# Optimization experiments

Measured on AMD Instinct MI355X. Metric: run time of the kernel, lower is better.

The kernel has to match this reference:

```python
import jax, jax.numpy as jnp
import numpy as np

N = 50000      # n_nodes
S = 16         # neighbors per node
D_IN = 256     # raw feature dim
PREP = 128     # prep_len
H = 2          # n_head
OUT = 64       # per-head spec output_dim (concat_node doubles it)
MP = 2         # n_mp (metapaths)
IN2 = 2 * OUT * H  # layer-2 input dim = 256


def setup_inputs() -> dict:
    key = jax.random.key(0)
    ks = jax.random.split(key, 7)
    feats = jax.random.normal(ks[0], (N, D_IN), jnp.float32)
    prep_W = jax.random.normal(ks[1], (D_IN, PREP), jnp.float32) * 0.05
    Wx1 = jax.random.normal(ks[2], (MP, H, PREP, OUT), jnp.float32) * 0.05
    Wn1 = jax.random.normal(ks[3], (MP, H, PREP, OUT), jnp.float32) * 0.05
    Wx2 = jax.random.normal(ks[4], (MP, H, IN2, OUT), jnp.float32) * 0.05
    Wn2 = jax.random.normal(ks[5], (MP, H, IN2, OUT), jnp.float32) * 0.05
    node_neigh = jax.random.randint(ks[6], (MP, N, S), 0, N, dtype=jnp.int32)
    return {"feats": feats, "prep_W": prep_W, "Wx1": Wx1, "Wn1": Wn1,
            "Wx2": Wx2, "Wn2": Wn2, "node_neigh": node_neigh}


def _agg_layer(x, neigh, Wx, Wn):
    # x: [N, d]; neigh: [N, S]; Wx, Wn: [H, d, OUT]
    # neighbor gather + mean (the chunk_edge = all_feats[node_neigh] path)
    agg = jnp.mean(x[neigh], axis=1)                  # [N, d]
    xh = jnp.einsum('nd,hdo->nho', x, Wx)             # [N, H, OUT]
    nh = jnp.einsum('nd,hdo->nho', agg, Wn)           # [N, H, OUT]
    h = jax.nn.relu(jnp.concatenate([xh, nh], -1))    # per-head concat_node
    return h.reshape(x.shape[0], -1)                  # heads concatenated


def reference(feats, prep_W, Wx1, Wn1, Wx2, Wn2, node_neigh):
    # feats[all_ids].detach() in the original -> stop_gradient
    feats = jax.lax.stop_gradient(feats)
    outs = []
    for mp in range(MP):
        h0 = feats @ prep_W                           # prep (dummy == layer-1 prep here)
        neigh = node_neigh[mp]
        h1 = _agg_layer(h0, neigh, Wx1[mp], Wn1[mp])  # [N, 256]
        h2 = _agg_layer(h1, neigh, Wx2[mp], Wn2[mp])  # [N, 256]
        outs.append(jnp.concatenate([h1, h2], axis=-1))  # skip-buffer concat
    return jnp.stack(outs, axis=0)                    # [MP, N, 512]
```

## Files before the change

kernel.cpp:

```cpp
#include <hip/hip_runtime.h>

#define NN 50000
#define SNEI 16
#define GB 782

typedef unsigned short ushort_t;
typedef unsigned int uint_t;
typedef unsigned long long u64;
typedef __attribute__((ext_vector_type(8))) short bhalf8;
typedef __attribute__((ext_vector_type(4))) float facc4;

__device__ __forceinline__ float b2f(uint_t u) {
    union { uint_t u; float f; } x; x.u = u << 16; return x.f;
}
__device__ __forceinline__ ushort_t f2b(float f) {
    union { float f; uint_t u; } x; x.f = f;
    return (ushort_t)((x.u + 0x7FFFu + ((x.u >> 16) & 1u)) >> 16);
}
__device__ __forceinline__ u64 pack4(float a, float b, float c, float d) {
    return (u64)f2b(a) | ((u64)f2b(b) << 16) | ((u64)f2b(c) << 32) | ((u64)f2b(d) << 48);
}

typedef const __attribute__((address_space(1))) void cglb_t;
typedef __attribute__((address_space(3))) void lds3_t;
__device__ __forceinline__ void gload16(const void* g, void* l) {
    __builtin_amdgcn_global_load_lds((cglb_t*)g, (lds3_t*)l, 16, 0, 0);
}

__global__ void permSetup(const float* __restrict__ prepW,
                          const float* __restrict__ Wx1, const float* __restrict__ Wn1,
                          const float* __restrict__ Wx2, const float* __restrict__ Wn2,
                          ushort_t* __restrict__ dst)
{
    int e = blockIdx.x * 256 + threadIdx.x;
    int q8 = e >> 3, j = e & 7;
    int layer = q8 >> 14;
    int qq = q8 & 16383;
    int mp = qq >> 13, isN = (qq >> 12) & 1, q = qq & 4095;
    int lane = q & 63, nf = (q >> 6) & 7, ks = q >> 9;
    int c = nf * 16 + (lane & 15);
    int k = ks * 32 + ((lane >> 4) << 3) + j;
    float v;
    if (layer == 0) {
        const float* W1 = (isN ? Wn1 : Wx1) + mp * 16384 + (c >> 6) * 8192 + (c & 63);
        const float* pw = prepW + (size_t)k * 128;
        float s = 0.f;
#pragma unroll 8
        for (int p = 0; p < 128; ++p) s += pw[p] * W1[(size_t)p * 64];
        v = s;
    } else {
        const float* W2 = (isN ? Wn2 : Wx2) + mp * 32768 + (c >> 6) * 16384 + (size_t)k * 64 + (c & 63);
        v = *W2;
    }
    dst[(size_t)q8 * 8 + j] = f2b(v);
}

template<bool XF32, bool L1>
__global__ __launch_bounds__(256, 4)
void proj_gemm(const void* __restrict__ Xv, size_t xStr,
               const ushort_t* __restrict__ W, size_t wStr,
               float* __restrict__ out, size_t oStr,
               ushort_t* __restrict__ h1, size_t hStr,
               ushort_t* __restrict__ P, size_t PStr)
{
    __shared__ bhalf8 lds[2560];
    u64* l64 = (u64*)lds;
    const int tid = threadIdx.x;
    const int lane = tid & 63;
    const int wid = tid >> 6;
    const int wave_m = wid >> 1, wave_n = wid & 1;
    const int m0 = blockIdx.x * 64;
    const int mp = blockIdx.y;

    const ushort_t* wx = W + (size_t)mp * wStr;
    const ushort_t* wn = wx + 4096 * 8;
    const float*    Xf = (const float*)Xv    + (size_t)mp * xStr;
    const ushort_t* Xb = (const ushort_t*)Xv + (size_t)mp * xStr;
    float* outp = out + (size_t)mp * oStr;
    ushort_t* h1p = L1 ? (h1 + (size_t)mp * hStr) : nullptr;
    ushort_t* Pp  = P + (size_t)mp * PStr;

    facc4 acc[2][8];
    const facc4 z = {0.f, 0.f, 0.f, 0.f};
#pragma unroll
    for (int i = 0; i < 2; ++i)
#pragma unroll
        for (int j = 0; j < 8; ++j) acc[i][j] = z;

    for (int kt = 0; kt < 4; ++kt) {
        if constexpr (XF32) {
#pragma unroll
            for (int it = 0; it < 2; ++it) {
                int s = tid + it * 256;
                int fp = s >> 6, ls = s & 63;
                int mf = fp & 3, ksl = fp >> 2;
                int grow = m0 + mf * 16 + (ls & 15); if (grow > NN - 1) grow = NN - 1;
                const float* gp = Xf + (size_t)grow * 256 + kt * 64 + ksl * 32 + ((ls >> 4) << 3);
                float4 f0 = *(const float4*)gp, f1 = *(const float4*)(gp + 4);
                l64[s * 2]     = pack4(f0.x, f0.y, f0.z, f0.w);
                l64[s * 2 + 1] = pack4(f1.x, f1.y, f1.z, f1.w);
            }
        } else {
#pragma unroll
            for (int it = 0; it < 2; ++it) {
                int u = wid + it * 4;
                int mf = u & 3, ksl = u >> 2;
                int grow = m0 + mf * 16 + (lane & 15); if (grow > NN - 1) grow = NN - 1;
                const ushort_t* src = Xb + (size_t)grow * 256 + kt * 64 + ksl * 32 + ((lane >> 4) << 3);
                gload16(src, (char*)lds + (u * 64 + lane) * 16);
            }
        }
#pragma unroll
        for (int it = 0; it < 4; ++it) {
            int cb = (it * 4 + wid) * 64;
            gload16(wx + ((size_t)kt * 1024 + cb + lane) * 8,
                    (char*)lds + (512 + cb + lane) * 16);
            gload16(wn + ((size_t)kt * 1024 + cb + lane) * 8,
                    (char*)lds + (1536 + cb + lane) * 16);
        }
        __syncthreads();
        const int wB = wave_n ? 1536 : 512;
#pragma unroll
        for (int ksl = 0; ksl < 2; ++ksl) {
            bhalf8 a0 = lds[(ksl * 4 + wave_m * 2 + 0) * 64 + lane];
            bhalf8 a1 = lds[(ksl * 4 + wave_m * 2 + 1) * 64 + lane];
#pragma unroll
            for (int nf = 0; nf < 8; ++nf) {
                bhalf8 b = lds[wB + (ksl * 8 + nf) * 64 + lane];
                acc[0][nf] = __builtin_amdgcn_mfma_f32_16x16x32_bf16(a0, b, acc[0][nf], 0, 0, 0);
                acc[1][nf] = __builtin_amdgcn_mfma_f32_16x16x32_bf16(a1, b, acc[1][nf], 0, 0, 0);
            }
        }
        __syncthreads();
    }
    const int cl = lane & 15, rg = lane >> 4;
    const int obase = L1 ? 0 : 256;
#pragma unroll
    for (int mf2 = 0; mf2 < 2; ++mf2) {
        int rowb = m0 + (wave_m * 2 + mf2) * 16 + rg * 4;
#pragma unroll
        for (int nf = 0; nf < 8; ++nf) {
            int cpr = nf * 16 + cl;
            int icol = (cpr >> 6) * 128 + (cpr & 63);
            facc4 v = acc[mf2][nf];
#pragma unroll
            for (int rr = 0; rr < 4; ++rr) {
                int row = rowb + rr;
                if (row < NN) {
                    if (wave_n == 0) {
                        float f = fmaxf(v[rr], 0.0f);
                        outp[(size_t)row * 512 + obase + icol] = f;
                        if constexpr (L1)
                            h1p[(size_t)row * 256 + icol] = f2b(f);
                    } else {
                        Pp[(size_t)row * 128 + cpr] = f2b(v[rr]);
                    }
                }
            }
        }
    }
}

template<bool L1>
__global__ __launch_bounds__(256)
void gatherK(const ushort_t* __restrict__ P, size_t PStr,
             const int* __restrict__ nb, size_t nStr,
             float* __restrict__ out, size_t oStr,
             ushort_t* __restrict__ h1, size_t hStr)
{
    const int mp = blockIdx.y;
    const ushort_t* Pp = P + (size_t)mp * PStr;
    const int* nbp = nb + (size_t)mp * nStr;
    float* outp = out + (size_t)mp * oStr;

    __shared__ int nls[256];
    const int nodeBase = blockIdx.x * 16;
    nls[threadIdx.x] = nbp[(size_t)nodeBase * SNEI + threadIdx.x];
    __syncthreads();

    const int nl = threadIdx.x >> 4, c = threadIdx.x & 15;
    const int node = nodeBase + nl;
    const int* nr = nls + nl * SNEI;
    float a0=0.f,a1=0.f,a2=0.f,a3=0.f,a4=0.f,a5=0.f,a6=0.f,a7=0.f;
#pragma unroll
    for (int s = 0; s < SNEI; ++s) {
        uint4 v = *(const uint4*)(Pp + (size_t)nr[s] * 128 + c * 8);
        a0 += b2f(v.x & 0xFFFFu); a1 += b2f(v.x >> 16);
        a2 += b2f(v.y & 0xFFFFu); a3 += b2f(v.y >> 16);
        a4 += b2f(v.z & 0xFFFFu); a5 += b2f(v.z >> 16);
        a6 += b2f(v.w & 0xFFFFu); a7 += b2f(v.w >> 16);
    }
    const float M = 0.0625f;
    float r0 = fmaxf(a0*M, 0.f), r1 = fmaxf(a1*M, 0.f);
    float r2 = fmaxf(a2*M, 0.f), r3 = fmaxf(a3*M, 0.f);
    float r4 = fmaxf(a4*M, 0.f), r5 = fmaxf(a5*M, 0.f);
    float r6 = fmaxf(a6*M, 0.f), r7 = fmaxf(a7*M, 0.f);
    const int head = c >> 3, off = (c & 7) * 8;
    const int obase = L1 ? 0 : 256;
    float* o = outp + (size_t)node * 512 + obase + head * 128 + 64 + off;
    *(float4*)o       = make_float4(r0, r1, r2, r3);
    *(float4*)(o + 4) = make_float4(r4, r5, r6, r7);
    if constexpr (L1) {
        ushort_t* hp = h1 + (size_t)mp * hStr + (size_t)node * 256 + head * 128 + 64 + off;
        *(u64*)hp       = pack4(r0, r1, r2, r3);
        *(u64*)(hp + 4) = pack4(r4, r5, r6, r7);
    }
}

extern "C" void kernel_launch(void* const* d_in, const int* in_sizes, int n_in,
                              void* d_out, int out_size, void* d_ws, size_t ws_size,
                              hipStream_t stream)
{
    const float* feats  = (const float*)d_in[0];
    const float* prepWp = (const float*)d_in[1];
    const float* Wx1    = (const float*)d_in[2];
    const float* Wn1    = (const float*)d_in[3];
    const float* Wx2    = (const float*)d_in[4];
    const float* Wn2    = (const float*)d_in[5];
    const int*   neigh  = (const int*)d_in[6];
    float* out = (float*)d_out;
    ushort_t* ws = (ushort_t*)d_ws;

    const size_t permElems = 262144;
    const size_t needBatched = permElems * 2
        + 2 * ((size_t)NN * 128 * 2 + (size_t)NN * 256 * 2);
    const bool batched = ws_size >= needBatched;
    const int nmp = batched ? 2 : 1;

    ushort_t* perm = ws;
    ushort_t* P    = ws + permElems;
    ushort_t* h1   = P + (size_t)nmp * NN * 128;

    permSetup<<<1024, 256, 0, stream>>>(prepWp, Wx1, Wn1, Wx2, Wn2, perm);

    const size_t PStr = batched ? (size_t)NN * 128 : 0;
    const size_t hStr = batched ? (size_t)NN * 256 : 0;
    const size_t oStr = batched ? (size_t)NN * 512 : 0;
    const size_t nStr = batched ? (size_t)NN * SNEI : 0;
    const size_t wStr = batched ? (size_t)8192 * 8 : 0;
    const int passes = batched ? 1 : 2;

    for (int p = 0; p < passes; ++p) {
        const ushort_t* w1 = perm + (size_t)p * 8192 * 8;
        const ushort_t* w2 = perm + (size_t)(16384 + p * 8192) * 8;
        float* outp = out + (size_t)p * NN * 512;
        const int* nbp = neigh + (size_t)p * NN * SNEI;
        dim3 gp(GB, nmp), gg(NN / 16, nmp);

        proj_gemm<true, true><<<gp, 256, 0, stream>>>(
            feats, 0, w1, wStr, outp, oStr, h1, hStr, P, PStr);
        gatherK<true><<<gg, 256, 0, stream>>>(
            P, PStr, nbp, nStr, outp, oStr, h1, hStr);
        proj_gemm<false, false><<<gp, 256, 0, stream>>>(
            h1, hStr, w2, wStr, outp, oStr, nullptr, 0, P, PStr);
        gatherK<false><<<gg, 256, 0, stream>>>(
            P, PStr, nbp, nStr, outp, oStr, nullptr, 0);
    }
}
```

Baseline: 193.2 us.

## Slice projected neighbor table by 32-column chunks for cache-friendlier gather

The projected neighbor features P are now stored as four column slices of 32 bf16 values per node instead of 128-wide rows. The gather kernel gets a slice grid dimension, so each block reads only 64-byte rows from one 3.2MB slice. That slice is more likely to stay resident in L2/LLC during the random neighbor gather. Each block now handles 64 nodes with a vectorized, clamped neighbor-index load, and the setup dot product uses two accumulators. The trade-off is that each neighbor index is read four times, once per slice, and output writes become narrower strided chunks.

```diff
diff --git a/kernel.cpp b/kernel.cpp
--- a/kernel.cpp
+++ b/kernel.cpp
@@ -44,10 +44,13 @@
     if (layer == 0) {
         const float* W1 = (isN ? Wn1 : Wx1) + mp * 16384 + (c >> 6) * 8192 + (c & 63);
         const float* pw = prepW + (size_t)k * 128;
-        float s = 0.f;
-#pragma unroll 8
-        for (int p = 0; p < 128; ++p) s += pw[p] * W1[(size_t)p * 64];
-        v = s;
+        float s0 = 0.f, s1 = 0.f;
+#pragma unroll 4
+        for (int p = 0; p < 128; p += 2) {
+            s0 += pw[p]     * W1[(size_t)p * 64];
+            s1 += pw[p + 1] * W1[(size_t)(p + 1) * 64];
+        }
+        v = s0 + s1;
     } else {
         const float* W2 = (isN ? Wn2 : Wx2) + mp * 32768 + (c >> 6) * 16384 + (size_t)k * 64 + (c & 63);
         v = *W2;
@@ -153,7 +156,7 @@
                         if constexpr (L1)
                             h1p[(size_t)row * 256 + icol] = f2b(f);
                     } else {
-                        Pp[(size_t)row * 128 + cpr] = f2b(v[rr]);
+                        Pp[(size_t)(cpr >> 5) * (NN * 32) + (size_t)row * 32 + (cpr & 31)] = f2b(v[rr]);
                     }
                 }
             }
@@ -163,28 +166,35 @@
 
 template<bool L1>
 __global__ __launch_bounds__(256)
-void gatherK(const ushort_t* __restrict__ P, size_t PStr,
+void gatherS(const ushort_t* __restrict__ P, size_t PStr,
              const int* __restrict__ nb, size_t nStr,
              float* __restrict__ out, size_t oStr,
              ushort_t* __restrict__ h1, size_t hStr)
 {
-    const int mp = blockIdx.y;
-    const ushort_t* Pp = P + (size_t)mp * PStr;
+    const int slice = blockIdx.y;
+    const int mp = blockIdx.z;
+    const ushort_t* Pp = P + (size_t)mp * PStr + (size_t)slice * (NN * 32);
     const int* nbp = nb + (size_t)mp * nStr;
     float* outp = out + (size_t)mp * oStr;
 
-    __shared__ int nls[256];
-    const int nodeBase = blockIdx.x * 16;
-    nls[threadIdx.x] = nbp[(size_t)nodeBase * SNEI + threadIdx.x];
+    __shared__ int nls[1024];
+    const int nodeBase = blockIdx.x * 64;
+    {
+        int i4 = nodeBase * 4 + threadIdx.x;
+        int mx = NN * 4 - 1;
+        if (i4 > mx) i4 = mx;
+        ((int4*)nls)[threadIdx.x] = ((const int4*)nbp)[i4];
+    }
     __syncthreads();
 
-    const int nl = threadIdx.x >> 4, c = threadIdx.x & 15;
+    const int nl = threadIdx.x >> 2, q = threadIdx.x & 3;
     const int node = nodeBase + nl;
+    if (node >= NN) return;
     const int* nr = nls + nl * SNEI;
     float a0=0.f,a1=0.f,a2=0.f,a3=0.f,a4=0.f,a5=0.f,a6=0.f,a7=0.f;
 #pragma unroll
     for (int s = 0; s < SNEI; ++s) {
-        uint4 v = *(const uint4*)(Pp + (size_t)nr[s] * 128 + c * 8);
+        uint4 v = *(const uint4*)(Pp + (size_t)nr[s] * 32 + q * 8);
         a0 += b2f(v.x & 0xFFFFu); a1 += b2f(v.x >> 16);
         a2 += b2f(v.y & 0xFFFFu); a3 += b2f(v.y >> 16);
         a4 += b2f(v.z & 0xFFFFu); a5 += b2f(v.z >> 16);
@@ -195,13 +205,14 @@
     float r2 = fmaxf(a2*M, 0.f), r3 = fmaxf(a3*M, 0.f);
     float r4 = fmaxf(a4*M, 0.f), r5 = fmaxf(a5*M, 0.f);
     float r6 = fmaxf(a6*M, 0.f), r7 = fmaxf(a7*M, 0.f);
-    const int head = c >> 3, off = (c & 7) * 8;
+    const int head = slice >> 1;
+    const int coff = head * 128 + 64 + (slice & 1) * 32 + q * 8;
     const int obase = L1 ? 0 : 256;
-    float* o = outp + (size_t)node * 512 + obase + head * 128 + 64 + off;
+    float* o = outp + (size_t)node * 512 + obase + coff;
     *(float4*)o       = make_float4(r0, r1, r2, r3);
     *(float4*)(o + 4) = make_float4(r4, r5, r6, r7);
     if constexpr (L1) {
-        ushort_t* hp = h1 + (size_t)mp * hStr + (size_t)node * 256 + head * 128 + 64 + off;
+        ushort_t* hp = h1 + (size_t)mp * hStr + (size_t)node * 256 + coff;
         *(u64*)hp       = pack4(r0, r1, r2, r3);
         *(u64*)(hp + 4) = pack4(r4, r5, r6, r7);
     }
@@ -245,15 +256,15 @@
         const ushort_t* w2 = perm + (size_t)(16384 + p * 8192) * 8;
         float* outp = out + (size_t)p * NN * 512;
         const int* nbp = neigh + (size_t)p * NN * SNEI;
-        dim3 gp(GB, nmp), gg(NN / 16, nmp);
+        dim3 gp(GB, nmp), gg(GB, 4, nmp);
 
         proj_gemm<true, true><<<gp, 256, 0, stream>>>(
             feats, 0, w1, wStr, outp, oStr, h1, hStr, P, PStr);
-        gatherK<true><<<gg, 256, 0, stream>>>(
+        gatherS<true><<<gg, 256, 0, stream>>>(
             P, PStr, nbp, nStr, outp, oStr, h1, hStr);
         proj_gemm<false, false><<<gp, 256, 0, stream>>>(
             h1, hStr, w2, wStr, outp, oStr, nullptr, 0, P, PStr);
-        gatherK<false><<<gg, 256, 0, stream>>>(
+        gatherS<false><<<gg, 256, 0, stream>>>(
             P, PStr, nbp, nStr, outp, oStr, nullptr, 0);
     }
 }
```

Result: no change. 195.1 us (+1.0%).
